# Kernel tuning notes

Hardware: AMD Instinct MI355X
Metric: run time of the kernel (lower is better)

The kernel has to match this reference:

```python
import jax, jax.numpy as jnp
import numpy as np
from jax import lax

B, C, H, W = 8, 128, 128, 128
K = 3
RED = 8

def setup_inputs() -> dict:
    key = jax.random.key(0)
    ks = jax.random.split(key, 8)
    s = 0.05
    return {
        "x": jax.random.normal(ks[0], (B, C, H, W), dtype=jnp.float32),
        "altitude": jax.random.normal(ks[1], (B, 128), dtype=jnp.float32),
        "W1": jax.random.normal(ks[2], (128, 128), dtype=jnp.float32) * s,          # Linear(128,128), no bias
        "W2": jax.random.normal(ks[3], (128 * K * K, 128), dtype=jnp.float32) * s,  # Linear(128,128*k*k)
        "conv_w": jax.random.normal(ks[4], (C, C), dtype=jnp.float32) * s,          # 1x1 conv weight [out,in]
        "conv_b": jax.random.normal(ks[5], (C,), dtype=jnp.float32) * s,
        "ca_w1": jax.random.normal(ks[6], (C // RED, C), dtype=jnp.float32) * s,    # CA squeeze 1x1 conv
        "ca_w2": jax.random.normal(ks[7], (C, C // RED), dtype=jnp.float32) * s,    # CA excite 1x1 conv
    }

def reference(x, altitude, W1, W2, conv_w, conv_b, ca_w1, ca_w2):
    b, c, h, w = x.shape
    # kernel generator MLP: [b,128] -> [b, 128*K*K] -> (b*c, 1, K, K)
    feat = jax.nn.leaky_relu(altitude @ W1.T, negative_slope=0.1)
    kern = (feat @ W2.T).reshape(b * c, 1, K, K)
    # per-sample, per-channel conv: groups = b*c (pure generated depthwise)
    pad = (K - 1) // 2
    xr = x.reshape(1, b * c, h, w)
    out = lax.conv_general_dilated(
        xr, kern, window_strides=(1, 1), padding=[(pad, pad), (pad, pad)],
        dimension_numbers=("NCHW", "OIHW", "NCHW"), feature_group_count=b * c)
    out = jax.nn.relu(out).reshape(b, c, h, w)
    # 1x1 pointwise conv
    out = jnp.einsum("bchw,oc->bohw", out, conv_w) + conv_b[None, :, None, None]
    # channel attention from altitude
    a1 = jax.nn.leaky_relu(altitude @ ca_w1.T, negative_slope=0.1)
    att = jax.nn.sigmoid(a1 @ ca_w2.T)  # [b, c]
    return out + x * att[:, :, None, None]
```

## Files before the change

### kernel.cpp

```cpp
#include <hip/hip_runtime.h>
#include <math.h>

typedef __attribute__((ext_vector_type(8))) __bf16 bf16x8;
typedef __attribute__((ext_vector_type(4))) __bf16 bf16x4;
typedef __attribute__((ext_vector_type(4))) float f32x4;

#define PLANE 16384
#define ROWW 128


__global__ __launch_bounds__(256) void precompute_kernel(
    const float* __restrict__ altitude,
    const float* __restrict__ W1,
    const float* __restrict__ W2,
    const float* __restrict__ ca_w1,
    const float* __restrict__ ca_w2,
    const float* __restrict__ conv_w,
    float* __restrict__ ws)
{
    int bid = blockIdx.x;
    int b = bid >> 2;
    int q = bid & 3;
    int t = threadIdx.x;
    __shared__ float alt_s[128];
    __shared__ float feat_s[128];
    __shared__ float a1_s[16];

    if (t < 128) alt_s[t] = altitude[b * 128 + t];
    __syncthreads();

    if (t < 128) {
        float s = 0.f;
        const float* wrow = W1 + t * 128;
        for (int j = 0; j < 128; ++j) s += alt_s[j] * wrow[j];
        feat_s[t] = (s >= 0.f) ? s : 0.1f * s;
    } else if (t < 144 && q == 1) {
        int r = t - 128;
        float s = 0.f;
        const float* wrow = ca_w1 + r * 128;
        for (int j = 0; j < 128; ++j) s += alt_s[j] * wrow[j];
        a1_s[r] = (s >= 0.f) ? s : 0.1f * s;
    }
    __syncthreads();

    for (int i = t; i < 288; i += 256) {
        int m = q * 288 + i;
        float s = 0.f;
        const float* wrow = W2 + m * 128;
        for (int j = 0; j < 128; ++j) s += feat_s[j] * wrow[j];
        int c = m / 9, k = m % 9;
        ws[b * 1536 + c * 12 + k] = s;
    }
    if (q == 1 && t < 128) {
        float s = 0.f;
        const float* wrow = ca_w2 + t * 16;
        for (int r = 0; r < 16; ++r) s += a1_s[r] * wrow[r];
        ws[12288 + b * 128 + t] = 1.f / (1.f + expf(-s));
    }
    if (q == 2 && t < 256) {
        int kc   = t >> 6;
        int lane = t & 63;
        int o  = b * 16 + (lane & 15);
        int cb = kc * 32 + 8 * (lane >> 4);
        bf16x8 v;
        #pragma unroll
        for (int j = 0; j < 8; ++j)
            v[j] = (__bf16)conv_w[o * 128 + cb + j];
        ushort* wf = (ushort*)(ws + 13312);
        *reinterpret_cast<bf16x8*>(wf + ((size_t)(b * 4 + kc) * 64 + lane) * 8) = v;
    }
}

__global__ __launch_bounds__(512, 8) void fused_kernel(
    const float* __restrict__ x,
    const float* __restrict__ conv_b,
    const float* __restrict__ ws,
    float* __restrict__ out)
{
    const float* __restrict__ kern_w = ws;
    const float* __restrict__ att_w  = ws + 12288;
    const ushort* __restrict__ wfrag = (const ushort*)(ws + 13312);

    int bid = blockIdx.x;
    int b = bid & 7;
    int h = bid >> 3;

    __shared__ __align__(16) ushort dwT[128 * 136];
    __shared__ __align__(16) float ktaps[128 * 12];

    int t = threadIdx.x;
    const float* __restrict__ xb = x + (size_t)b * 128 * PLANE;

    for (int i = t; i < 384; i += 512) {
        float4 v = *(const float4*)(kern_w + b * 1536 + i * 4);
        *(float4*)(&ktaps[i * 4]) = v;
    }
    __syncthreads();

    {
        int pg = t & 15;
        int cg = t >> 4;
        int gp0 = pg * 8;
        int c0 = cg * 4;

        int   rT = (h > 0)   ? h - 1 : h;
        int   rB = (h < 127) ? h + 1 : h;
        float mT = (h > 0)   ? 1.f : 0.f;
        float mB = (h < 127) ? 1.f : 0.f;
        float mL = (pg > 0)  ? 1.f : 0.f;
        float mR = (pg < 15) ? 1.f : 0.f;

        bf16x4 bv0, bv1, bv2, bv3, bv4, bv5, bv6, bv7;

#define ROWACC(A, B, KL, KC, KR) {                                     \
        float l_ = __shfl_up((B).w, 1) * mL;                           \
        float r_ = __shfl_down((A).x, 1) * mR;                         \
        o0 = fmaf((KL), l_,    fmaf((KC), (A).x, fmaf((KR), (A).y, o0))); \
        o1 = fmaf((KL), (A).x, fmaf((KC), (A).y, fmaf((KR), (A).z, o1))); \
        o2 = fmaf((KL), (A).y, fmaf((KC), (A).z, fmaf((KR), (A).w, o2))); \
        o3 = fmaf((KL), (A).z, fmaf((KC), (A).w, fmaf((KR), (B).x, o3))); \
        o4 = fmaf((KL), (A).w, fmaf((KC), (B).x, fmaf((KR), (B).y, o4))); \
        o5 = fmaf((KL), (B).x, fmaf((KC), (B).y, fmaf((KR), (B).z, o5))); \
        o6 = fmaf((KL), (B).y, fmaf((KC), (B).z, fmaf((KR), (B).w, o6))); \
        o7 = fmaf((KL), (B).z, fmaf((KC), (B).w, fmaf((KR), r_,    o7))); }

#define DW_CH(CI) {                                                    \
        const float* q_ = xb + (size_t)(c0 + (CI)) * PLANE;            \
        const float* pT = q_ + rT * ROWW + gp0;                        \
        const float* pC = q_ + h  * ROWW + gp0;                        \
        const float* pB = q_ + rB * ROWW + gp0;                        \
        float4 aT = *(const float4*)pT, bT = *(const float4*)(pT + 4); \
        float4 aC = *(const float4*)pC, bC = *(const float4*)(pC + 4); \
        float4 aB = *(const float4*)pB, bB = *(const float4*)(pB + 4); \
        const float* tp = ktaps + (c0 + (CI)) * 12;                    \
        float4 kA = *(const float4*)tp;                                \
        float4 kB = *(const float4*)(tp + 4);                          \
        float  k8v = tp[8];                                            \
        float k0 = kA.x * mT, k1 = kA.y * mT, k2 = kA.z * mT;          \
        float k3 = kA.w,      k4 = kB.x,      k5 = kB.y;               \
        float k6 = kB.z * mB, k7 = kB.w * mB, k8 = k8v * mB;           \
        float o0 = 0.f, o1 = 0.f, o2 = 0.f, o3 = 0.f;                  \
        float o4 = 0.f, o5 = 0.f, o6 = 0.f, o7 = 0.f;                  \
        ROWACC(aT, bT, k0, k1, k2)                                     \
        ROWACC(aC, bC, k3, k4, k5)                                     \
        ROWACC(aB, bB, k6, k7, k8)                                     \
        bv0[(CI)] = (__bf16)fmaxf(o0, 0.f);                            \
        bv1[(CI)] = (__bf16)fmaxf(o1, 0.f);                            \
        bv2[(CI)] = (__bf16)fmaxf(o2, 0.f);                            \
        bv3[(CI)] = (__bf16)fmaxf(o3, 0.f);                            \
        bv4[(CI)] = (__bf16)fmaxf(o4, 0.f);                            \
        bv5[(CI)] = (__bf16)fmaxf(o5, 0.f);                            \
        bv6[(CI)] = (__bf16)fmaxf(o6, 0.f);                            \
        bv7[(CI)] = (__bf16)fmaxf(o7, 0.f); }

        DW_CH(0) DW_CH(1) DW_CH(2) DW_CH(3)
#undef DW_CH
#undef ROWACC

        int slotoff = (((cg >> 1) ^ pg) * 8) + ((cg & 1) * 4);
#define ST(J) *reinterpret_cast<bf16x4*>(&dwT[(pg * 8 + (J)) * 136 + slotoff]) = bv##J;
        ST(0) ST(1) ST(2) ST(3) ST(4) ST(5) ST(6) ST(7)
#undef ST
    }
    __syncthreads();
    __builtin_amdgcn_sched_barrier(0);

    {
        int w    = t >> 6;
        int lane = t & 63;
        int r = lane & 15;
        int g = lane >> 4;

        bf16x8 bfr[4];
        #pragma unroll
        for (int kc = 0; kc < 4; ++kc)
            bfr[kc] = *reinterpret_cast<const bf16x8*>(
                wfrag + ((size_t)(w * 4 + kc) * 64 + lane) * 8);

        f32x4 acc[8];
        #pragma unroll
        for (int pt = 0; pt < 8; ++pt) acc[pt] = (f32x4){0.f, 0.f, 0.f, 0.f};

        #pragma unroll
        for (int pt = 0; pt < 8; ++pt) {
            int px = pt * 16 + r;
            int srow = px * 136;
            int s2 = px >> 3;
            #pragma unroll
            for (int kc = 0; kc < 4; ++kc) {
                bf16x8 a = *reinterpret_cast<const bf16x8*>(
                    &dwT[srow + (((kc * 4 + g) ^ s2) * 8)]);
                acc[pt] = __builtin_amdgcn_mfma_f32_16x16x32_bf16(a, bfr[kc], acc[pt], 0, 0, 0);
            }
        }

        int o = w * 16 + r;
        float bi = conv_b[o];
        float at = att_w[b * 128 + o];
        size_t rowoff = (size_t)(b * 128 + o) * PLANE + (size_t)h * ROWW;
        const float* xrow = x + rowoff;
        float* orow = out + rowoff;
        #pragma unroll
        for (int pt = 0; pt < 8; ++pt) {
            int px = pt * 16 + g * 4;
            float4 xv = *(const float4*)(xrow + px);
            float4 ov;
            ov.x = acc[pt][0] + bi + xv.x * at;
            ov.y = acc[pt][1] + bi + xv.y * at;
            ov.z = acc[pt][2] + bi + xv.z * at;
            ov.w = acc[pt][3] + bi + xv.w * at;
            *(float4*)(orow + px) = ov;
        }
    }
}

extern "C" void kernel_launch(void* const* d_in, const int* in_sizes, int n_in,
                              void* d_out, int out_size, void* d_ws, size_t ws_size,
                              hipStream_t stream) {
    (void)in_sizes; (void)n_in; (void)out_size; (void)ws_size;
    const float* x        = (const float*)d_in[0];
    const float* altitude = (const float*)d_in[1];
    const float* W1       = (const float*)d_in[2];
    const float* W2       = (const float*)d_in[3];
    const float* conv_w   = (const float*)d_in[4];
    const float* conv_b   = (const float*)d_in[5];
    const float* ca_w1    = (const float*)d_in[6];
    const float* ca_w2    = (const float*)d_in[7];
    float* out = (float*)d_out;
    float* ws  = (float*)d_ws;

    hipLaunchKernelGGL(precompute_kernel, dim3(32), dim3(256), 0, stream,
                       altitude, W1, W2, ca_w1, ca_w2, conv_w, ws);
    hipLaunchKernelGGL(fused_kernel, dim3(1024), dim3(512), 0, stream,
                       x, conv_b, ws, out);
}
```

Baseline: 48.77 us.

## Process two output rows per block to reuse halo rows and weight fragments

Each block now computes two adjacent image rows instead of one, loading four input rows per channel instead of six across two blocks. This cuts redundant halo reads of x and amortizes the tap and MFMA weight-fragment loads over twice the work. The x residual loads are also hoisted ahead of the MFMA loop. In exchange the grid halves to 512 blocks, LDS per block roughly doubles, register pressure rises, and the launch bound drops occupancy to 4 blocks per CU.

New measurement: 44.78 us (median of 2 runs). 8.2% less time.

```diff
diff --git a/kernel.cpp b/kernel.cpp
--- a/kernel.cpp
+++ b/kernel.cpp
@@ -71,7 +71,7 @@
     }
 }
 
-__global__ __launch_bounds__(512, 8) void fused_kernel(
+__global__ __launch_bounds__(512, 4) void fused_kernel(
     const float* __restrict__ x,
     const float* __restrict__ conv_b,
     const float* __restrict__ ws,
@@ -82,10 +82,11 @@
     const ushort* __restrict__ wfrag = (const ushort*)(ws + 13312);
 
     int bid = blockIdx.x;
-    int b = bid & 7;
-    int h = bid >> 3;
-
-    __shared__ __align__(16) ushort dwT[128 * 136];
+    int b  = bid & 7;
+    int rb = bid >> 3;
+    int h0 = rb * 2;
+
+    __shared__ __align__(16) ushort dwT[2][128 * 136];
     __shared__ __align__(16) float ktaps[128 * 12];
 
     int t = threadIdx.x;
@@ -103,63 +104,85 @@
         int gp0 = pg * 8;
         int c0 = cg * 4;
 
-        int   rT = (h > 0)   ? h - 1 : h;
-        int   rB = (h < 127) ? h + 1 : h;
-        float mT = (h > 0)   ? 1.f : 0.f;
-        float mB = (h < 127) ? 1.f : 0.f;
         float mL = (pg > 0)  ? 1.f : 0.f;
         float mR = (pg < 15) ? 1.f : 0.f;
-
-        bf16x4 bv0, bv1, bv2, bv3, bv4, bv5, bv6, bv7;
-
-#define ROWACC(A, B, KL, KC, KR) {                                     \
-        float l_ = __shfl_up((B).w, 1) * mL;                           \
-        float r_ = __shfl_down((A).x, 1) * mR;                         \
-        o0 = fmaf((KL), l_,    fmaf((KC), (A).x, fmaf((KR), (A).y, o0))); \
+        float mTop = (rb > 0)  ? 1.f : 0.f;
+        float mBot = (rb < 63) ? 1.f : 0.f;
+        int r0 = (rb > 0)  ? h0 - 1 : h0;
+        int r3 = (rb < 63) ? h0 + 2 : h0;
+
+        bf16x4 bv[2][8];
+
+#define NEIGH(A, B, LV, RV) \
+        float LV = __shfl_up((B).w, 1) * mL; \
+        float RV = __shfl_down((A).x, 1) * mR;
+
+#define ROWACC(A, B, LV, RV, KL, KC, KR) {                                \
+        o0 = fmaf((KL), LV,    fmaf((KC), (A).x, fmaf((KR), (A).y, o0))); \
         o1 = fmaf((KL), (A).x, fmaf((KC), (A).y, fmaf((KR), (A).z, o1))); \
         o2 = fmaf((KL), (A).y, fmaf((KC), (A).z, fmaf((KR), (A).w, o2))); \
         o3 = fmaf((KL), (A).z, fmaf((KC), (A).w, fmaf((KR), (B).x, o3))); \
         o4 = fmaf((KL), (A).w, fmaf((KC), (B).x, fmaf((KR), (B).y, o4))); \
         o5 = fmaf((KL), (B).x, fmaf((KC), (B).y, fmaf((KR), (B).z, o5))); \
         o6 = fmaf((KL), (B).y, fmaf((KC), (B).z, fmaf((KR), (B).w, o6))); \
-        o7 = fmaf((KL), (B).z, fmaf((KC), (B).w, fmaf((KR), r_,    o7))); }
+        o7 = fmaf((KL), (B).z, fmaf((KC), (B).w, fmaf((KR), RV,    o7))); }
 
 #define DW_CH(CI) {                                                    \
         const float* q_ = xb + (size_t)(c0 + (CI)) * PLANE;            \
-        const float* pT = q_ + rT * ROWW + gp0;                        \
-        const float* pC = q_ + h  * ROWW + gp0;                        \
-        const float* pB = q_ + rB * ROWW + gp0;                        \
-        float4 aT = *(const float4*)pT, bT = *(const float4*)(pT + 4); \
-        float4 aC = *(const float4*)pC, bC = *(const float4*)(pC + 4); \
-        float4 aB = *(const float4*)pB, bB = *(const float4*)(pB + 4); \
+        const float* p0_ = q_ + r0 * ROWW + gp0;                       \
+        const float* p1_ = q_ + h0 * ROWW + gp0;                       \
+        const float* p2_ = q_ + (h0 + 1) * ROWW + gp0;                 \
+        const float* p3_ = q_ + r3 * ROWW + gp0;                       \
+        float4 a0 = *(const float4*)p0_, b0 = *(const float4*)(p0_ + 4); \
+        float4 a1 = *(const float4*)p1_, b1 = *(const float4*)(p1_ + 4); \
+        float4 a2 = *(const float4*)p2_, b2 = *(const float4*)(p2_ + 4); \
+        float4 a3 = *(const float4*)p3_, b3 = *(const float4*)(p3_ + 4); \
+        NEIGH(a0, b0, l0, rr0) NEIGH(a1, b1, l1, rr1)                  \
+        NEIGH(a2, b2, l2, rr2) NEIGH(a3, b3, l3, rr3)                  \
         const float* tp = ktaps + (c0 + (CI)) * 12;                    \
         float4 kA = *(const float4*)tp;                                \
         float4 kB = *(const float4*)(tp + 4);                          \
         float  k8v = tp[8];                                            \
-        float k0 = kA.x * mT, k1 = kA.y * mT, k2 = kA.z * mT;          \
-        float k3 = kA.w,      k4 = kB.x,      k5 = kB.y;               \
-        float k6 = kB.z * mB, k7 = kB.w * mB, k8 = k8v * mB;           \
-        float o0 = 0.f, o1 = 0.f, o2 = 0.f, o3 = 0.f;                  \
-        float o4 = 0.f, o5 = 0.f, o6 = 0.f, o7 = 0.f;                  \
-        ROWACC(aT, bT, k0, k1, k2)                                     \
-        ROWACC(aC, bC, k3, k4, k5)                                     \
-        ROWACC(aB, bB, k6, k7, k8)                                     \
-        bv0[(CI)] = (__bf16)fmaxf(o0, 0.f);                            \
-        bv1[(CI)] = (__bf16)fmaxf(o1, 0.f);                            \
-        bv2[(CI)] = (__bf16)fmaxf(o2, 0.f);                            \
-        bv3[(CI)] = (__bf16)fmaxf(o3, 0.f);                            \
-        bv4[(CI)] = (__bf16)fmaxf(o4, 0.f);                            \
-        bv5[(CI)] = (__bf16)fmaxf(o5, 0.f);                            \
-        bv6[(CI)] = (__bf16)fmaxf(o6, 0.f);                            \
-        bv7[(CI)] = (__bf16)fmaxf(o7, 0.f); }
+        {            \
+            float o0 = 0.f, o1 = 0.f, o2 = 0.f, o3 = 0.f;              \
+            float o4 = 0.f, o5 = 0.f, o6 = 0.f, o7 = 0.f;              \
+            ROWACC(a0, b0, l0, rr0, kA.x * mTop, kA.y * mTop, kA.z * mTop) \
+            ROWACC(a1, b1, l1, rr1, kA.w, kB.x, kB.y)                  \
+            ROWACC(a2, b2, l2, rr2, kB.z, kB.w, k8v)                   \
+            bv[0][0][(CI)] = (__bf16)fmaxf(o0, 0.f);                   \
+            bv[0][1][(CI)] = (__bf16)fmaxf(o1, 0.f);                   \
+            bv[0][2][(CI)] = (__bf16)fmaxf(o2, 0.f);                   \
+            bv[0][3][(CI)] = (__bf16)fmaxf(o3, 0.f);                   \
+            bv[0][4][(CI)] = (__bf16)fmaxf(o4, 0.f);                   \
+            bv[0][5][(CI)] = (__bf16)fmaxf(o5, 0.f);                   \
+            bv[0][6][(CI)] = (__bf16)fmaxf(o6, 0.f);                   \
+            bv[0][7][(CI)] = (__bf16)fmaxf(o7, 0.f);                   \
+        }                                                              \
+        {         \
+            float o0 = 0.f, o1 = 0.f, o2 = 0.f, o3 = 0.f;              \
+            float o4 = 0.f, o5 = 0.f, o6 = 0.f, o7 = 0.f;              \
+            ROWACC(a1, b1, l1, rr1, kA.x, kA.y, kA.z)                  \
+            ROWACC(a2, b2, l2, rr2, kA.w, kB.x, kB.y)                  \
+            ROWACC(a3, b3, l3, rr3, kB.z * mBot, kB.w * mBot, k8v * mBot) \
+            bv[1][0][(CI)] = (__bf16)fmaxf(o0, 0.f);                   \
+            bv[1][1][(CI)] = (__bf16)fmaxf(o1, 0.f);                   \
+            bv[1][2][(CI)] = (__bf16)fmaxf(o2, 0.f);                   \
+            bv[1][3][(CI)] = (__bf16)fmaxf(o3, 0.f);                   \
+            bv[1][4][(CI)] = (__bf16)fmaxf(o4, 0.f);                   \
+            bv[1][5][(CI)] = (__bf16)fmaxf(o5, 0.f);                   \
+            bv[1][6][(CI)] = (__bf16)fmaxf(o6, 0.f);                   \
+            bv[1][7][(CI)] = (__bf16)fmaxf(o7, 0.f);                   \
+        } }
 
         DW_CH(0) DW_CH(1) DW_CH(2) DW_CH(3)
 #undef DW_CH
 #undef ROWACC
+#undef NEIGH
 
         int slotoff = (((cg >> 1) ^ pg) * 8) + ((cg & 1) * 4);
-#define ST(J) *reinterpret_cast<bf16x4*>(&dwT[(pg * 8 + (J)) * 136 + slotoff]) = bv##J;
-        ST(0) ST(1) ST(2) ST(3) ST(4) ST(5) ST(6) ST(7)
+#define ST(RW, J) *reinterpret_cast<bf16x4*>(&dwT[RW][(pg * 8 + (J)) * 136 + slotoff]) = bv[RW][J];
+        ST(0,0) ST(0,1) ST(0,2) ST(0,3) ST(0,4) ST(0,5) ST(0,6) ST(0,7)
+        ST(1,0) ST(1,1) ST(1,2) ST(1,3) ST(1,4) ST(1,5) ST(1,6) ST(1,7)
 #undef ST
     }
     __syncthreads();
@@ -177,39 +200,49 @@
             bfr[kc] = *reinterpret_cast<const bf16x8*>(
                 wfrag + ((size_t)(w * 4 + kc) * 64 + lane) * 8);
 
-        f32x4 acc[8];
-        #pragma unroll
-        for (int pt = 0; pt < 8; ++pt) acc[pt] = (f32x4){0.f, 0.f, 0.f, 0.f};
-
-        #pragma unroll
-        for (int pt = 0; pt < 8; ++pt) {
-            int px = pt * 16 + r;
-            int srow = px * 136;
-            int s2 = px >> 3;
-            #pragma unroll
-            for (int kc = 0; kc < 4; ++kc) {
-                bf16x8 a = *reinterpret_cast<const bf16x8*>(
-                    &dwT[srow + (((kc * 4 + g) ^ s2) * 8)]);
-                acc[pt] = __builtin_amdgcn_mfma_f32_16x16x32_bf16(a, bfr[kc], acc[pt], 0, 0, 0);
-            }
-        }
-
         int o = w * 16 + r;
         float bi = conv_b[o];
         float at = att_w[b * 128 + o];
-        size_t rowoff = (size_t)(b * 128 + o) * PLANE + (size_t)h * ROWW;
-        const float* xrow = x + rowoff;
-        float* orow = out + rowoff;
-        #pragma unroll
-        for (int pt = 0; pt < 8; ++pt) {
-            int px = pt * 16 + g * 4;
-            float4 xv = *(const float4*)(xrow + px);
-            float4 ov;
-            ov.x = acc[pt][0] + bi + xv.x * at;
-            ov.y = acc[pt][1] + bi + xv.y * at;
-            ov.z = acc[pt][2] + bi + xv.z * at;
-            ov.w = acc[pt][3] + bi + xv.w * at;
-            *(float4*)(orow + px) = ov;
+
+        #pragma unroll 1
+        for (int r2 = 0; r2 < 2; ++r2) {
+            const ushort* plane = dwT[r2];
+            size_t rowoff = (size_t)(b * 128 + o) * PLANE + (size_t)(h0 + r2) * ROWW;
+            const float* xrow = x + rowoff;
+            float* orow = out + rowoff;
+
+            float4 xv[8];
+            #pragma unroll
+            for (int pt = 0; pt < 8; ++pt)
+                xv[pt] = *(const float4*)(xrow + pt * 16 + g * 4);
+
+            f32x4 acc[8];
+            #pragma unroll
+            for (int pt = 0; pt < 8; ++pt) acc[pt] = (f32x4){0.f, 0.f, 0.f, 0.f};
+
+            #pragma unroll
+            for (int pt = 0; pt < 8; ++pt) {
+                int px = pt * 16 + r;
+                int srow = px * 136;
+                int s2 = px >> 3;
+                #pragma unroll
+                for (int kc = 0; kc < 4; ++kc) {
+                    bf16x8 a = *reinterpret_cast<const bf16x8*>(
+                        &plane[srow + (((kc * 4 + g) ^ s2) * 8)]);
+                    acc[pt] = __builtin_amdgcn_mfma_f32_16x16x32_bf16(a, bfr[kc], acc[pt], 0, 0, 0);
+                }
+            }
+
+            #pragma unroll
+            for (int pt = 0; pt < 8; ++pt) {
+                int px = pt * 16 + g * 4;
+                float4 ov;
+                ov.x = acc[pt][0] + bi + xv[pt].x * at;
+                ov.y = acc[pt][1] + bi + xv[pt].y * at;
+                ov.z = acc[pt][2] + bi + xv[pt].z * at;
+                ov.w = acc[pt][3] + bi + xv[pt].w * at;
+                *(float4*)(orow + px) = ov;
+            }
         }
     }
 }
@@ -231,6 +264,6 @@
 
     hipLaunchKernelGGL(precompute_kernel, dim3(32), dim3(256), 0, stream,
                        altitude, W1, W2, ca_w1, ca_w2, conv_w, ws);
-    hipLaunchKernelGGL(fused_kernel, dim3(1024), dim3(512), 0, stream,
+    hipLaunchKernelGGL(fused_kernel, dim3(512), dim3(512), 0, stream,
                        x, conv_b, ws, out);
 }
```
